# Kernel tuning notes

Hardware: AMD Instinct MI355X
Metric: run time of the kernel (lower is better)

Reference implementation:

```python
import jax, jax.numpy as jnp
import numpy as np

N = 20000      # nodes
E = 1280000    # edges
F = 42         # num_features (forced equal to mpnn out_channels by the code)
H = 20         # lstm hidden per direction


def setup_inputs() -> dict:
    key = jax.random.key(0)
    ks = jax.random.split(key, 17)
    def rn(k, shape, sc=0.1):
        return jax.random.normal(k, shape, dtype=jnp.float32) * sc
    return {
        "x": rn(ks[0], (N, F), 1.0),
        "edge_index": jax.random.randint(ks[1], (2, E), 0, N),
        "edge_attr": jax.random.uniform(ks[2], (E, 1), dtype=jnp.float32),
        "lin_w": rn(ks[3], (F, 2 * F)),
        "lin_b": rn(ks[4], (F,)),
        "gru_w_ih": rn(ks[5], (3 * F, F)),
        "gru_w_hh": rn(ks[6], (3 * F, F)),
        "gru_b_ih": rn(ks[7], (3 * F,)),
        "gru_b_hh": rn(ks[8], (3 * F,)),
        "lstm_w_ih_f": rn(ks[9], (4 * H, F)),
        "lstm_w_hh_f": rn(ks[10], (4 * H, H)),
        "lstm_b_f": rn(ks[11], (4 * H,)),
        "lstm_w_ih_b": rn(ks[12], (4 * H, F)),
        "lstm_w_hh_b": rn(ks[13], (4 * H, H)),
        "lstm_b_b": rn(ks[14], (4 * H,)),
        "cls_w": rn(ks[15], (1, 2 * H)),
        "cls_b": rn(ks[16], (1,)),
    }


def _lstm_dir(xs, w_ih, w_hh, b):
    # xs: [N, F] treated as a length-N sequence with batch 1
    x_proj = xs @ w_ih.T + b  # [N, 4H] precompute input contribution
    def cell(carry, xp):
        h, c = carry
        g = xp + w_hh @ h                      # [4H]
        i, f, gg, o = jnp.split(g, 4)
        c = jax.nn.sigmoid(f) * c + jax.nn.sigmoid(i) * jnp.tanh(gg)
        h = jax.nn.sigmoid(o) * jnp.tanh(c)
        return (h, c), h
    h0 = jnp.zeros((H,), xs.dtype)
    _, hs = jax.lax.scan(cell, (h0, h0), x_proj)
    return hs  # [N, H]


def reference(x, edge_index, edge_attr, lin_w, lin_b,
              gru_w_ih, gru_w_hh, gru_b_ih, gru_b_hh,
              lstm_w_ih_f, lstm_w_hh_f, lstm_b_f,
              lstm_w_ih_b, lstm_w_hh_b, lstm_b_b,
              cls_w, cls_b):
    n = x.shape[0]
    src, dst = edge_index[0], edge_index[1]
    # --- message: gather x_i (target) / x_j (source), concat-linear, sigmoid gate
    x_i = x[dst]                               # [E, F]
    x_j = x[src]                               # [E, F]
    msg = jnp.concatenate([x_i, x_j], axis=1) @ lin_w.T + lin_b  # [E, F]
    msg = msg * jax.nn.sigmoid(-edge_attr)     # gate on -time_diff, broadcast [E,1]
    # --- aggregate: scatter-add at target nodes
    agg = jax.ops.segment_sum(msg, dst, num_segments=n)  # [N, F]
    # --- GRU, seq_len=1, batch=N, input = hidden init = agg
    gi = agg @ gru_w_ih.T + gru_b_ih           # [N, 3F]
    gh = agg @ gru_w_hh.T + gru_b_hh           # [N, 3F]
    i_r, i_z, i_n = jnp.split(gi, 3, axis=1)
    h_r, h_z, h_n = jnp.split(gh, 3, axis=1)
    r = jax.nn.sigmoid(i_r + h_r)
    z = jax.nn.sigmoid(i_z + h_z)
    ng = jnp.tanh(i_n + r * h_n)
    hx = (1.0 - z) * ng + z * agg              # [N, F]
    # --- bidirectional LSTM over nodes as a sequence (batch=1)
    h_fwd = _lstm_dir(hx, lstm_w_ih_f, lstm_w_hh_f, lstm_b_f)                # [N, H]
    h_bwd = _lstm_dir(hx[::-1], lstm_w_ih_b, lstm_w_hh_b, lstm_b_b)[::-1]    # [N, H]
    h_cat = jnp.concatenate([h_fwd, h_bwd], axis=1)  # [N, 2H]
    return h_cat @ cls_w.T + cls_b             # [N, 1]
```

## Files before the change

kernel.cpp:

```cpp
#include <hip/hip_runtime.h>

#define NN 20000
#define EE 1280000
#define FF 42
#define HH 20
#define PSTR 44

#define CHUNK 8
#define WARM 24
#define NCHD 2500
#define TOTCH (2*NCHD)
#define LW 4
#define TT 16

#define NBIN 625
#define BINW 32
#define CAP  2560
#define NCHKB 160
#define CHKE 8000

#define WGROWS 168
#define WLROWS 160
#define WGTOT (WGROWS*PSTR)
#define WLTOT (WLROWS*PSTR)

#define NPB 1641
#define WPB 57

__device__ __forceinline__ float fexp2(float x){ return __builtin_amdgcn_exp2f(x); }
__device__ __forceinline__ float frcp(float x){ return __builtin_amdgcn_rcpf(x); }
__device__ __forceinline__ float fsigmoid(float x){ return frcp(1.f + fexp2(-1.442695041f*x)); }
__device__ __forceinline__ float ftanh(float x){ return 2.f*frcp(1.f + fexp2(-2.885390082f*x)) - 1.f; }

__global__ __launch_bounds__(256) void k_front(
    const float* __restrict__ x, const float* __restrict__ lw,
    const float* __restrict__ gwih, const float* __restrict__ gwhh,
    const float* __restrict__ lwihf, const float* __restrict__ lwihb,
    float* __restrict__ PA, float* __restrict__ PB,
    float* __restrict__ WG, float* __restrict__ WL,
    unsigned* __restrict__ gcur)
{
  __shared__ float2 w1S[FF*21];
  __shared__ float2 w2S[FF*21];
  int bid = blockIdx.x;
  if (bid < NPB){
    for (int idx=threadIdx.x; idx<FF*21; idx+=256){
      int k = idx/21, fp = idx - 21*k;
      w1S[idx] = make_float2(lw[(2*fp)*84 + k],      lw[(2*fp+1)*84 + k]);
      w2S[idx] = make_float2(lw[(2*fp)*84 + 42 + k], lw[(2*fp+1)*84 + 42 + k]);
    }
    __syncthreads();
    int tid = bid*256 + threadIdx.x;
    if (tid >= NN*21) return;
    int n = tid / 21;
    int fp = tid - n*21;
    const float* xr = x + n*FF;
    float2 pa = make_float2(0.f,0.f), pb = make_float2(0.f,0.f);
#pragma unroll 6
    for (int k=0;k<FF;k++){
      float xv = xr[k];
      float2 w1 = w1S[k*21+fp], w2 = w2S[k*21+fp];
      pa.x += w1.x*xv; pa.y += w1.y*xv;
      pb.x += w2.x*xv; pb.y += w2.y*xv;
    }
    ((float2*)(PA + n*PSTR))[fp] = pa;
    ((float2*)(PB + n*PSTR))[fp] = pb;
    if (fp == 0){
      PA[n*PSTR+42] = 0.f; PA[n*PSTR+43] = 0.f;
      PB[n*PSTR+42] = 0.f; PB[n*PSTR+43] = 0.f;
    }
  } else {
    int i = (bid - NPB)*256 + threadIdx.x;
    if (i < NBIN) gcur[i] = 0u;
    if (i < WGTOT){
      int r = i/PSTR, k = i - PSTR*r;
      float v = 0.f;
      if (k < FF){
        if (r < 84)       v = gwih[r*FF+k] + gwhh[r*FF+k];
        else if (r < 126) v = gwih[r*FF+k];
        else              v = gwhh[(r-42)*FF+k];
      }
      WG[i] = v;
    }
    int j = i - WGTOT;
    if (j >= 0 && j < WLTOT){
      int r = j/PSTR, k = j - PSTR*r;
      float v = 0.f;
      if (k < FF) v = (r < 80) ? lwihf[r*FF+k] : lwihb[(r-80)*FF+k];
      WL[j] = v;
    }
  }
}

__global__ __launch_bounds__(256) void k_bin(
    const int* __restrict__ src, const int* __restrict__ dst,
    const float* __restrict__ ea,
    unsigned* __restrict__ gcur, int2* __restrict__ binned)
{
  __shared__ unsigned h[NBIN];
  __shared__ unsigned base[NBIN];
  int blk = blockIdx.x, tid = threadIdx.x;
  for (int i=tid; i<NBIN; i+=256) h[i] = 0u;
  __syncthreads();
  const int* d = dst + blk*CHKE;
  for (int i=tid; i<CHKE; i+=256) atomicAdd(&h[d[i]>>5], 1u);
  __syncthreads();
  for (int i=tid; i<NBIN; i+=256){
    unsigned c = h[i];
    base[i] = c ? atomicAdd(&gcur[i], c) : 0u;
  }
  __syncthreads();
  for (int i=tid; i<NBIN; i+=256) h[i] = 0u;
  __syncthreads();
  for (int i=tid; i<CHKE; i+=256){
    int e = blk*CHKE + i;
    int dd = dst[e];
    int s  = src[e];
    float g = fsigmoid(-ea[e]);
    int b = dd >> 5;
    unsigned p = base[b] + atomicAdd(&h[b], 1u);
    if (p < CAP){
      int2 r; r.x = s | ((dd & 31) << 16); r.y = __float_as_int(g);
      binned[(long)b*CAP + p] = r;
    }
  }
}

__global__ __launch_bounds__(512, 8) void k_agg(
    const float* __restrict__ PA, const float* __restrict__ PB,
    const unsigned* __restrict__ gcur,
    const int2* __restrict__ binned, const float* __restrict__ lin_b,
    float* __restrict__ aggT)
{
  __shared__ int2 edS[CAP];
  __shared__ unsigned int cntL[BINW];
  __shared__ unsigned int offsN[BINW+1];
  __shared__ float lbS[PSTR];

  int b = blockIdx.x, tid = threadIdx.x;
  if (tid < PSTR) lbS[tid] = (tid < FF) ? lin_b[tid] : 0.f;
  int cl = (int)gcur[b]; if (cl > CAP) cl = CAP;
  long e0 = (long)b*CAP;

  int2 E[5];
  if (tid < BINW) cntL[tid] = 0;
  __syncthreads();
#pragma unroll
  for (int u=0; u<5; u++){
    int i = tid + u*512;
    if (i < cl){
      E[u] = binned[e0+i];
      atomicAdd(&cntL[E[u].x >> 16], 1u);
    }
  }
  __syncthreads();
  if (tid < 64){
    unsigned v = (tid < BINW) ? cntL[tid] : 0u;
    unsigned x = v;
#pragma unroll
    for (int off=1; off<32; off<<=1){
      unsigned y = __shfl_up(x, off);
      if ((tid & 63) >= off) x += y;
    }
    if (tid < BINW) offsN[tid+1] = x;
    if (tid == 0) offsN[0] = 0;
  }
  __syncthreads();
  if (tid < BINW) cntL[tid] = offsN[tid];
  __syncthreads();
#pragma unroll
  for (int u=0; u<5; u++){
    int i = tid + u*512;
    if (i < cl){
      unsigned p = atomicAdd(&cntL[E[u].x >> 16], 1u);
      edS[p] = E[u];
    }
  }
  __syncthreads();

  int w = tid >> 6, lane = tid & 63;
  int grp = lane / 11;
  int fp  = lane - grp*11;
  bool lact = grp < 5;
  unsigned a0[4], aE[4];
  int M = 0;
#pragma unroll
  for (int j=0;j<4;j++){
    int n = w + 8*j;
    a0[j] = offsN[n]; aE[j] = offsN[n+1];
    int len = (int)(aE[j]-a0[j]); if (len > M) M = len;
  }
  float4 acc[4]; float gs[4];
#pragma unroll
  for (int j=0;j<4;j++){ acc[j]=make_float4(0.f,0.f,0.f,0.f); gs[j]=0.f; }
  for (int t=0; t<M; t+=5){
    float4 pv[4]; float gv[4];
#pragma unroll
    for (int j=0;j<4;j++){
      unsigned k = a0[j] + (unsigned)(t + grp);
      bool v = lact && (k < aE[j]);
      unsigned ks = v ? k : 0u;
      int2 Ee = edS[ks];
      gv[j] = v ? __int_as_float(Ee.y) : 0.f;
      pv[j] = ((const float4*)(PB + (Ee.x & 0xFFFF)*PSTR))[fp];
    }
#pragma unroll
    for (int j=0;j<4;j++){
      acc[j].x += gv[j]*pv[j].x;  acc[j].y += gv[j]*pv[j].y;
      acc[j].z += gv[j]*pv[j].z;  acc[j].w += gv[j]*pv[j].w;
      gs[j]    += gv[j];
    }
  }
#pragma unroll
  for (int j=0;j<4;j++){
    float vx=acc[j].x, vy=acc[j].y, vz=acc[j].z, vw=acc[j].w, g=gs[j];
#pragma unroll
    for (int s=1;s<5;s++){
      vx += __shfl(acc[j].x, lane + 11*s);
      vy += __shfl(acc[j].y, lane + 11*s);
      vz += __shfl(acc[j].z, lane + 11*s);
      vw += __shfl(acc[j].w, lane + 11*s);
      g  += __shfl(gs[j],    lane + 11*s);
    }
    if (lane < 11){
      int gn = b*BINW + w + 8*j;
      const float4 pa = ((const float4*)(PA + (long)gn*PSTR))[fp];
      float4 lb = ((const float4*)lbS)[fp];
      int c0 = 4*fp;
      aggT[(long)(c0+0)*NN + gn] = (pa.x + lb.x)*g + vx;
      aggT[(long)(c0+1)*NN + gn] = (pa.y + lb.y)*g + vy;
      if (c0+2 < FF) aggT[(long)(c0+2)*NN + gn] = (pa.z + lb.z)*g + vz;
      if (c0+3 < FF) aggT[(long)(c0+3)*NN + gn] = (pa.w + lb.w)*g + vw;
    }
  }
}

__global__ __launch_bounds__(256) void k_gruF(
    const float* __restrict__ aggT,
    const float* __restrict__ WG,
    const float* __restrict__ gbih, const float* __restrict__ gbhh,
    float* __restrict__ hxT)
{
  int n = blockIdx.x*256 + threadIdx.x;
  int j0 = 2*blockIdx.y, j1 = j0 + 1;
  if (n >= NN) return;
  const float* wr0 = WG + j0*PSTR;
  const float* wz0 = WG + (42+j0)*PSTR;
  const float* wi0 = WG + (84+j0)*PSTR;
  const float* wh0 = WG + (126+j0)*PSTR;
  const float* wr1 = WG + j1*PSTR;
  const float* wz1 = WG + (42+j1)*PSTR;
  const float* wi1 = WG + (84+j1)*PSTR;
  const float* wh1 = WG + (126+j1)*PSTR;
  float sR0 = gbih[j0]+gbhh[j0], sZ0 = gbih[42+j0]+gbhh[42+j0];
  float sI0 = gbih[84+j0],       sH0 = gbhh[84+j0];
  float sR1 = gbih[j1]+gbhh[j1], sZ1 = gbih[42+j1]+gbhh[42+j1];
  float sI1 = gbih[84+j1],       sH1 = gbhh[84+j1];
#pragma unroll
  for (int k=0; k<FF; k++){
    float a = aggT[(long)k*NN + n];
    sR0 += wr0[k]*a; sZ0 += wz0[k]*a; sI0 += wi0[k]*a; sH0 += wh0[k]*a;
    sR1 += wr1[k]*a; sZ1 += wz1[k]*a; sI1 += wi1[k]*a; sH1 += wh1[k]*a;
  }
  float r0 = fsigmoid(sR0), z0 = fsigmoid(sZ0);
  float ng0 = ftanh(sI0 + r0*sH0);
  hxT[(long)j0*NN + n] = (1.f - z0)*ng0 + z0*aggT[(long)j0*NN + n];
  float r1 = fsigmoid(sR1), z1 = fsigmoid(sZ1);
  float ng1 = ftanh(sI1 + r1*sH1);
  hxT[(long)j1*NN + n] = (1.f - z1)*ng1 + z1*aggT[(long)j1*NN + n];
}

__global__ __launch_bounds__(256) void k_projF(
    const float* __restrict__ hxT,
    const float* __restrict__ WL,
    const float* __restrict__ lbf, const float* __restrict__ lbb,
    float* __restrict__ xpf, float* __restrict__ xpb)
{
  int n = blockIdx.x*256 + threadIdx.x;
  int gq = blockIdx.y;
  if (n >= NN) return;
  bool fw = gq < 20;
  int g0 = 4*gq;
  int gl = fw ? gq : gq - 20;
  int gr = fw ? g0 : g0 - 80;
  const float* w0 = WL + (g0+0)*PSTR;
  const float* w1 = WL + (g0+1)*PSTR;
  const float* w2 = WL + (g0+2)*PSTR;
  const float* w3 = WL + (g0+3)*PSTR;
  const float* bb = fw ? lbf : lbb;
  float a0 = bb[gr+0], a1 = bb[gr+1], a2 = bb[gr+2], a3 = bb[gr+3];
#pragma unroll
  for (int k=0; k<FF; k++){
    float h = hxT[(long)k*NN + n];
    a0 += w0[k]*h; a1 += w1[k]*h; a2 += w2[k]*h; a3 += w3[k]*h;
  }
  float* xp = fw ? xpf : xpb;
  ((float4*)(xp + (long)n*80))[gl] = make_float4(a0, a1, a2, a3);
}

__global__ __launch_bounds__(256) void k_lstm(
    const float* __restrict__ xpf, const float* __restrict__ xpb,
    const float* __restrict__ whhf, const float* __restrict__ whhb,
    float* __restrict__ hf, float* __restrict__ hb)
{
  __shared__ float bufAll[LW][2][TT*80];
  int wv = threadIdx.x >> 6;
  int lane = threadIdx.x & 63;
  int c = blockIdx.x*LW + wv;
  if (c >= TOTCH) return;
  int dir = (c >= NCHD) ? 1 : 0;
  int chunk = c - dir*NCHD;
  int p0 = chunk*CHUNK;
  if (p0 >= NN) return;
  int p1 = p0 + CHUNK; if (p1 > NN) p1 = NN;

  const float* xp  = dir ? xpb  : xpf;
  const float* whh = dir ? whhb : whhf;
  float* hout      = dir ? hb   : hf;
  float (*buf)[TT*80] = bufAll[wv];

  int m = lane & 31;
  int half = lane >> 5;
  int mm = (m < HH) ? m : HH-1;
  int rowA = half*40 + mm;
  int rowB = rowA + HH;
  float2 WA[10], WB[10];
#pragma unroll
  for (int kk=0;kk<10;kk++){
    WA[kk] = make_float2(whh[rowA*HH+2*kk], whh[rowA*HH+2*kk+1]);
    WB[kk] = make_float2(whh[rowB*HH+2*kk], whh[rowB*HH+2*kk+1]);
  }
  const float cE = half ? -2.885390082f : -1.442695041f;
  const float cM = half ? 2.f : 1.f;
  const float cA = half ? -1.f : 0.f;
  int colA = rowA;
  int colB = rowB;

  int ps = (p0 >= WARM) ? (p0-WARM) : 0;
  int steps = p1 - ps;
  int ntiles = (steps + TT - 1)/TT;

  float4 R0,R1,R2,R3,R4;
  auto fetch = [&](int j){
    int a = ps + j*TT;
    long g0;
    if (!dir) g0 = (long)a*80;
    else { int t_lo = NN - a - TT; if (t_lo < 0) t_lo = 0; g0 = (long)t_lo*80; }
    const float* s = xp + g0 + lane*4;
    R0 = *(const float4*)(s);
    R1 = *(const float4*)(s + 256);
    R2 = *(const float4*)(s + 512);
    R3 = *(const float4*)(s + 768);
    R4 = *(const float4*)(s + 1024);
  };
  auto stash = [&](int dbuf){
    float* d = buf[dbuf] + lane*4;
    *(float4*)(d)        = R0;
    *(float4*)(d + 256)  = R1;
    *(float4*)(d + 512)  = R2;
    *(float4*)(d + 768)  = R3;
    *(float4*)(d + 1024) = R4;
  };

  fetch(0); stash(0);
  if (ntiles > 1) fetch(1);

  float c2 = 0.f, h = 0.f;
  float2 H[10];
#pragma unroll
  for (int kk=0;kk<10;kk++) H[kk] = make_float2(0.f, 0.f);

  int t_lo0 = 0;
  if (dir){ t_lo0 = NN - ps - TT; if (t_lo0 < 0) t_lo0 = 0; }
  int row0 = dir ? (NN-1-ps - t_lo0) : 0;
  float nxA = buf[0][row0*80 + colA];
  float nxB = buf[0][row0*80 + colB];

  for (int j=0; j<ntiles; ++j){
    if (j+1 < ntiles) stash((j+1)&1);
    if (j+2 < ntiles) fetch(j+2);
    const float* B  = buf[j&1];
    const float* Bn = buf[(j+1)&1];
    int a = ps + j*TT;
    int t_lo = 0;
    if (dir){ t_lo = NN - a - TT; if (t_lo < 0) t_lo = 0; }
    int aN = a + TT;
    int t_loN = 0;
    if (dir){ t_loN = NN - aN - TT; if (t_loN < 0) t_loN = 0; }
#pragma unroll 4
    for (int r=0; r<TT; ++r){
      int p = a + r;
      float xA = nxA, xB = nxB;
      if (r+1 < TT){
        int rowN = dir ? (NN-1-(p+1) - t_lo) : (r+1);
        if (p+1 < ps+steps || !dir){
          nxA = B[rowN*80 + colA];
          nxB = B[rowN*80 + colB];
        }
      } else if (j+1 < ntiles){
        int rowN = dir ? (NN-1-aN - t_loN) : 0;
        nxA = Bn[rowN*80 + colA];
        nxB = Bn[rowN*80 + colB];
      }
      float aA0=xA, aA1=0.f, aB0=xB, aB1=0.f;
#pragma unroll
      for (int kk=0;kk<10;kk++){
        aA0 += WA[kk].x*H[kk].x;  aA1 += WA[kk].y*H[kk].y;
        aB0 += WB[kk].x*H[kk].x;  aB1 += WB[kk].y*H[kk].y;
      }
      float gA = aA0+aA1, gB = aB0+aB1;
      float actA = cM*frcp(1.f + fexp2(cE*gA)) + cA;
      float actB = frcp(1.f + fexp2(-1.442695041f*gB));
      float gT = __shfl_xor(actA, 32);
      float oT = __shfl_xor(actB, 32);
      c2 = actB*c2 + actA*gT;
      h = oT*ftanh(c2);
#pragma unroll
      for (int kk=0;kk<10;kk++){
        float va = __int_as_float(__builtin_amdgcn_readlane(__float_as_int(h), 2*kk));
        float vb = __int_as_float(__builtin_amdgcn_readlane(__float_as_int(h), 2*kk+1));
        H[kk] = make_float2(va, vb);
      }
      if (p >= p0 && p < p1 && lane < HH){
        int t = dir ? (NN-1-p) : p;
        hout[t*HH + lane] = h;
      }
    }
  }
}

__global__ __launch_bounds__(256) void k_cls(
    const float* __restrict__ hf, const float* __restrict__ hb,
    const float* __restrict__ cw, const float* __restrict__ cb,
    float* __restrict__ out)
{
  int n = blockIdx.x*256 + threadIdx.x;
  if (n >= NN) return;
  float s = cb[0];
  const float* hfr = hf + n*HH;
  const float* hbr = hb + n*HH;
#pragma unroll
  for (int k=0;k<HH;k++){
    s += hfr[k]*cw[k] + hbr[k]*cw[HH+k];
  }
  out[n] = s;
}

extern "C" void kernel_launch(void* const* d_in, const int* in_sizes, int n_in,
                              void* d_out, int out_size, void* d_ws, size_t ws_size,
                              hipStream_t stream) {
  (void)in_sizes; (void)n_in; (void)out_size; (void)ws_size;
  const float* x      = (const float*)d_in[0];
  const int*   ei     = (const int*)  d_in[1];
  const float* ea     = (const float*)d_in[2];
  const float* lin_w  = (const float*)d_in[3];
  const float* lin_b  = (const float*)d_in[4];
  const float* gwih   = (const float*)d_in[5];
  const float* gwhh   = (const float*)d_in[6];
  const float* gbih   = (const float*)d_in[7];
  const float* gbhh   = (const float*)d_in[8];
  const float* lwihf  = (const float*)d_in[9];
  const float* lwhhf  = (const float*)d_in[10];
  const float* lbf    = (const float*)d_in[11];
  const float* lwihb  = (const float*)d_in[12];
  const float* lwhhb  = (const float*)d_in[13];
  const float* lbb    = (const float*)d_in[14];
  const float* cw     = (const float*)d_in[15];
  const float* cb     = (const float*)d_in[16];
  float* out = (float*)d_out;

  const int* src = ei;
  const int* dst = ei + EE;

  float* PA     = (float*)d_ws;
  float* PB     = PA + NN*PSTR;
  float* xpf    = PB + NN*PSTR;
  float* xpb    = xpf + NN*80;
  float* hf     = xpb + NN*80;
  float* hb     = hf + NN*HH;
  float* WG     = hb + NN*HH;
  float* WL     = WG + WGTOT;
  float* aggT   = WL + WLTOT;
  float* hxT    = aggT + 42*NN;
  int2*  binned = (int2*)(hxT + 42*NN);
  unsigned* gcur = (unsigned*)(binned + (long)NBIN*CAP);

  k_front<<<NPB + WPB, 256, 0, stream>>>(x, lin_w, gwih, gwhh, lwihf, lwihb,
                                         PA, PB, WG, WL, gcur);
  k_bin<<<NCHKB, 256, 0, stream>>>(src, dst, ea, gcur, binned);
  k_agg<<<NBIN, 512, 0, stream>>>(PA, PB, gcur, binned, lin_b, aggT);
  k_gruF<<<dim3((NN + 255)/256, FF/2), 256, 0, stream>>>(aggT, WG, gbih, gbhh, hxT);
  k_projF<<<dim3((NN + 255)/256, 40), 256, 0, stream>>>(hxT, WL, lbf, lbb, xpf, xpb);
  k_lstm<<<(TOTCH + LW - 1)/LW, 256, 0, stream>>>(xpf, xpb, lwhhf, lwhhb, hf, hb);
  k_cls<<<(NN + 255)/256, 256, 0, stream>>>(hf, hb, cw, cb, out);
}
```

Measured before the change: 238.7 us.

## Replace two-level bin sort with per-node fixed-capacity edge buckets via global atomics

The edge binning changes from per-block LDS histograms over 32-node bins, followed by an in-LDS counting sort in the aggregation kernel, to direct global atomic slot claims per destination node with a fixed capacity of 128 edges per node. The aggregation kernel then builds offsets from the per-node counts and copies each node's bucket into shared memory, dropping the local re-sort and its atomics. This adds contention on 1.28M global atomics and scattered 8-byte writes. Edges beyond 128 per node are silently dropped, which is safe only if in-degree stays under the cap.

```diff
diff --git a/kernel.cpp b/kernel.cpp
--- a/kernel.cpp
+++ b/kernel.cpp
@@ -16,8 +16,7 @@
 #define NBIN 625
 #define BINW 32
 #define CAP  2560
-#define NCHKB 160
-#define CHKE 8000
+#define CAPN 128
 
 #define WGROWS 168
 #define WLROWS 160
@@ -25,7 +24,7 @@
 #define WLTOT (WLROWS*PSTR)
 
 #define NPB 1641
-#define WPB 57
+#define WPB 79
 
 __device__ __forceinline__ float fexp2(float x){ return __builtin_amdgcn_exp2f(x); }
 __device__ __forceinline__ float frcp(float x){ return __builtin_amdgcn_rcpf(x); }
@@ -38,7 +37,7 @@
     const float* __restrict__ lwihf, const float* __restrict__ lwihb,
     float* __restrict__ PA, float* __restrict__ PB,
     float* __restrict__ WG, float* __restrict__ WL,
-    unsigned* __restrict__ gcur)
+    unsigned* __restrict__ ncur)
 {
   __shared__ float2 w1S[FF*21];
   __shared__ float2 w2S[FF*21];
@@ -71,7 +70,7 @@
     }
   } else {
     int i = (bid - NPB)*256 + threadIdx.x;
-    if (i < NBIN) gcur[i] = 0u;
+    if (i < NN) ncur[i] = 0u;
     if (i < WGTOT){
       int r = i/PSTR, k = i - PSTR*r;
       float v = 0.f;
@@ -95,67 +94,42 @@
 __global__ __launch_bounds__(256) void k_bin(
     const int* __restrict__ src, const int* __restrict__ dst,
     const float* __restrict__ ea,
-    unsigned* __restrict__ gcur, int2* __restrict__ binned)
-{
-  __shared__ unsigned h[NBIN];
-  __shared__ unsigned base[NBIN];
-  int blk = blockIdx.x, tid = threadIdx.x;
-  for (int i=tid; i<NBIN; i+=256) h[i] = 0u;
-  __syncthreads();
-  const int* d = dst + blk*CHKE;
-  for (int i=tid; i<CHKE; i+=256) atomicAdd(&h[d[i]>>5], 1u);
-  __syncthreads();
-  for (int i=tid; i<NBIN; i+=256){
-    unsigned c = h[i];
-    base[i] = c ? atomicAdd(&gcur[i], c) : 0u;
-  }
-  __syncthreads();
-  for (int i=tid; i<NBIN; i+=256) h[i] = 0u;
-  __syncthreads();
-  for (int i=tid; i<CHKE; i+=256){
-    int e = blk*CHKE + i;
-    int dd = dst[e];
-    int s  = src[e];
-    float g = fsigmoid(-ea[e]);
-    int b = dd >> 5;
-    unsigned p = base[b] + atomicAdd(&h[b], 1u);
-    if (p < CAP){
-      int2 r; r.x = s | ((dd & 31) << 16); r.y = __float_as_int(g);
-      binned[(long)b*CAP + p] = r;
-    }
-  }
+    unsigned* __restrict__ ncur, int2* __restrict__ nodeEdges)
+{
+  int t = blockIdx.x*256 + threadIdx.x;
+  int4   d4 = ((const int4*)  dst)[t];
+  int4   s4 = ((const int4*)  src)[t];
+  float4 a4 = ((const float4*)ea )[t];
+  unsigned p;
+  p = atomicAdd(&ncur[d4.x], 1u);
+  if (p < CAPN) nodeEdges[(long)d4.x*CAPN + p] = make_int2(s4.x, __float_as_int(fsigmoid(-a4.x)));
+  p = atomicAdd(&ncur[d4.y], 1u);
+  if (p < CAPN) nodeEdges[(long)d4.y*CAPN + p] = make_int2(s4.y, __float_as_int(fsigmoid(-a4.y)));
+  p = atomicAdd(&ncur[d4.z], 1u);
+  if (p < CAPN) nodeEdges[(long)d4.z*CAPN + p] = make_int2(s4.z, __float_as_int(fsigmoid(-a4.z)));
+  p = atomicAdd(&ncur[d4.w], 1u);
+  if (p < CAPN) nodeEdges[(long)d4.w*CAPN + p] = make_int2(s4.w, __float_as_int(fsigmoid(-a4.w)));
 }
 
 __global__ __launch_bounds__(512, 8) void k_agg(
     const float* __restrict__ PA, const float* __restrict__ PB,
-    const unsigned* __restrict__ gcur,
-    const int2* __restrict__ binned, const float* __restrict__ lin_b,
+    const unsigned* __restrict__ ncur,
+    const int2* __restrict__ nodeEdges, const float* __restrict__ lin_b,
     float* __restrict__ aggT)
 {
   __shared__ int2 edS[CAP];
-  __shared__ unsigned int cntL[BINW];
   __shared__ unsigned int offsN[BINW+1];
   __shared__ float lbS[PSTR];
 
   int b = blockIdx.x, tid = threadIdx.x;
   if (tid < PSTR) lbS[tid] = (tid < FF) ? lin_b[tid] : 0.f;
-  int cl = (int)gcur[b]; if (cl > CAP) cl = CAP;
-  long e0 = (long)b*CAP;
-
-  int2 E[5];
-  if (tid < BINW) cntL[tid] = 0;
-  __syncthreads();
-#pragma unroll
-  for (int u=0; u<5; u++){
-    int i = tid + u*512;
-    if (i < cl){
-      E[u] = binned[e0+i];
-      atomicAdd(&cntL[E[u].x >> 16], 1u);
-    }
-  }
-  __syncthreads();
+
   if (tid < 64){
-    unsigned v = (tid < BINW) ? cntL[tid] : 0u;
+    unsigned v = 0u;
+    if (tid < BINW){
+      unsigned c = ncur[b*BINW + tid];
+      v = (c > CAPN) ? CAPN : c;
+    }
     unsigned x = v;
 #pragma unroll
     for (int off=1; off<32; off<<=1){
@@ -166,19 +140,22 @@
     if (tid == 0) offsN[0] = 0;
   }
   __syncthreads();
-  if (tid < BINW) cntL[tid] = offsN[tid];
+
+  int w = tid >> 6, lane = tid & 63;
+
+#pragma unroll
+  for (int j=0;j<4;j++){
+    int n = w + 8*j;
+    unsigned a0s = offsN[n], a1s = offsN[n+1];
+    unsigned len = a1s - a0s;
+    const int2* sp = nodeEdges + (long)(b*BINW + n)*CAPN;
+    for (unsigned i=lane; i<len; i+=64){
+      unsigned p = a0s + i;
+      if (p < CAP) edS[p] = sp[i];
+    }
+  }
   __syncthreads();
-#pragma unroll
-  for (int u=0; u<5; u++){
-    int i = tid + u*512;
-    if (i < cl){
-      unsigned p = atomicAdd(&cntL[E[u].x >> 16], 1u);
-      edS[p] = E[u];
-    }
-  }
-  __syncthreads();
-
-  int w = tid >> 6, lane = tid & 63;
+
   int grp = lane / 11;
   int fp  = lane - grp*11;
   bool lact = grp < 5;
@@ -188,6 +165,8 @@
   for (int j=0;j<4;j++){
     int n = w + 8*j;
     a0[j] = offsN[n]; aE[j] = offsN[n+1];
+    if (a0[j] > CAP) a0[j] = CAP;
+    if (aE[j] > CAP) aE[j] = CAP;
     int len = (int)(aE[j]-a0[j]); if (len > M) M = len;
   }
   float4 acc[4]; float gs[4];
@@ -482,13 +461,13 @@
   float* WL     = WG + WGTOT;
   float* aggT   = WL + WLTOT;
   float* hxT    = aggT + 42*NN;
-  int2*  binned = (int2*)(hxT + 42*NN);
-  unsigned* gcur = (unsigned*)(binned + (long)NBIN*CAP);
+  int2*  nodeEdges = (int2*)(hxT + 42*NN);
+  unsigned* ncur = (unsigned*)(nodeEdges + (long)NN*CAPN);
 
   k_front<<<NPB + WPB, 256, 0, stream>>>(x, lin_w, gwih, gwhh, lwihf, lwihb,
-                                         PA, PB, WG, WL, gcur);
-  k_bin<<<NCHKB, 256, 0, stream>>>(src, dst, ea, gcur, binned);
-  k_agg<<<NBIN, 512, 0, stream>>>(PA, PB, gcur, binned, lin_b, aggT);
+                                         PA, PB, WG, WL, ncur);
+  k_bin<<<EE/1024, 256, 0, stream>>>(src, dst, ea, ncur, nodeEdges);
+  k_agg<<<NBIN, 512, 0, stream>>>(PA, PB, ncur, nodeEdges, lin_b, aggT);
   k_gruF<<<dim3((NN + 255)/256, FF/2), 256, 0, stream>>>(aggT, WG, gbih, gbhh, hxT);
   k_projF<<<dim3((NN + 255)/256, 40), 256, 0, stream>>>(hxT, WL, lbf, lbb, xpf, xpb);
   k_lstm<<<(TOTCH + LW - 1)/LW, 256, 0, stream>>>(xpf, xpb, lwhhf, lwhhb, hf, hb);
```

After: 305.8 us. +28.1%, slower.
